# Optimization experiments

Measured on AMD Instinct MI355X. Metric: run time of the kernel, lower is better.

Reference implementation:

```python
import jax, jax.numpy as jnp
import numpy as np
import math

LN_EPS = 1e-5

def layer_norm(x, g, b):
    mu = jnp.mean(x, axis=-1, keepdims=True)
    var = jnp.mean(jnp.square(x - mu), axis=-1, keepdims=True)
    return (x - mu) * jax.lax.rsqrt(var + LN_EPS) * g + b

def positional_encoding(seq_len, d_model):
    pos = jnp.arange(seq_len, dtype=jnp.float32)[:, None]
    div = jnp.exp(jnp.arange(0, d_model, 2, dtype=jnp.float32) * (-math.log(10000.0) / d_model))
    ang = pos * div  # [S, D/2]
    # interleave: even indices sin, odd indices cos
    return jnp.stack([jnp.sin(ang), jnp.cos(ang)], axis=-1).reshape(seq_len, d_model)

def setup_inputs() -> dict:
    key = jax.random.key(0)
    V, D, H, L, F, B, S = 32000, 768, 12, 6, 3072, 4, 1024
    ks = jax.random.split(key, 12)
    s = 0.02
    inp = {
        'tokens': jax.random.randint(ks[0], (B, S), 0, V),
        'emb': jax.random.normal(ks[1], (V, D), jnp.float32) * s,
        'Wq': jax.random.normal(ks[2], (L, D, D), jnp.float32) * s,
        'bq': jnp.zeros((L, D), jnp.float32),
        'Wk': jax.random.normal(ks[3], (L, D, D), jnp.float32) * s,
        'bk': jnp.zeros((L, D), jnp.float32),
        'Wv': jax.random.normal(ks[4], (L, D, D), jnp.float32) * s,
        'bv': jnp.zeros((L, D), jnp.float32),
        'Wo': jax.random.normal(ks[5], (L, D, D), jnp.float32) * s,
        'bo': jnp.zeros((L, D), jnp.float32),
        'W1': jax.random.normal(ks[6], (L, D, F), jnp.float32) * s,
        'b1': jnp.zeros((L, F), jnp.float32),
        'W2': jax.random.normal(ks[7], (L, F, D), jnp.float32) * s,
        'b2': jnp.zeros((L, D), jnp.float32),
        'ln1_g': jnp.ones((L, D), jnp.float32), 'ln1_b': jnp.zeros((L, D), jnp.float32),
        'ln2_g': jnp.ones((L, D), jnp.float32), 'ln2_b': jnp.zeros((L, D), jnp.float32),
        'lnf_g': jnp.ones((D,), jnp.float32), 'lnf_b': jnp.zeros((D,), jnp.float32),
        'head_W': jax.random.normal(ks[8], (V, D), jnp.float32) * s,
    }
    return inp

def gpt_forward(tokens, emb, Wq, bq, Wk, bk, Wv, bv, Wo, bo, W1, b1, W2, b2,
                ln1_g, ln1_b, ln2_g, ln2_b, lnf_g, lnf_b, head_W):
    B, S = tokens.shape
    D = emb.shape[1]
    H = 12
    dk = D // H
    scale = 1.0 / math.sqrt(dk)
    causal = jnp.tril(jnp.ones((S, S), dtype=bool))  # [S,S]

    x = emb[tokens] + positional_encoding(S, D)  # [B,S,D]

    def block(x, p):
        wq, bq_, wk, bk_, wv, bv_, wo, bo_, w1, b1_, w2, b2_, g1, be1, g2, be2 = p
        h = layer_norm(x, g1, be1)
        q = (h @ wq + bq_).reshape(B, S, H, dk)
        k = (h @ wk + bk_).reshape(B, S, H, dk)
        v = (h @ wv + bv_).reshape(B, S, H, dk)
        scores = jnp.einsum('bqhd,bkhd->bhqk', q, k) * scale
        scores = jnp.where(causal, scores, -jnp.inf)
        attn = jax.nn.softmax(scores, axis=-1)
        o = jnp.einsum('bhqk,bkhd->bqhd', attn, v).reshape(B, S, D)
        x = x + o @ wo + bo_
        h2 = layer_norm(x, g2, be2)
        ff = jax.nn.gelu(h2 @ w1 + b1_, approximate=False) @ w2 + b2_
        x = x + ff
        return x, None

    layer_params = (Wq, bq, Wk, bk, Wv, bv, Wo, bo, W1, b1, W2, b2,
                    ln1_g, ln1_b, ln2_g, ln2_b)
    x, _ = jax.lax.scan(block, x, layer_params)
    x = layer_norm(x, lnf_g, lnf_b)
    logits = jnp.einsum('bsd,vd->bsv', x, head_W)  # head bias=False
    return logits

def reference(tokens, emb, Wq, bq, Wk, bk, Wv, bv, Wo, bo, W1, b1, W2, b2,
              ln1_g, ln1_b, ln2_g, ln2_b, lnf_g, lnf_b, head_W):
    return gpt_forward(tokens, emb, Wq, bq, Wk, bk, Wv, bv, Wo, bo, W1, b1, W2, b2,
                       ln1_g, ln1_b, ln2_g, ln2_b, lnf_g, lnf_b, head_W)
```

## Files before the change

kernel.cpp:

```cpp
#include <hip/hip_runtime.h>
#include <hip/hip_bf16.h>
#include <math.h>

#define BB 4
#define SS 1024
#define DD 768
#define HH 12
#define LL 6
#define FF 3072
#define VV 32000
#define DK 64
#define MM (BB * SS)

typedef __attribute__((ext_vector_type(8))) short s8v;
typedef __attribute__((ext_vector_type(4))) float f4v;

__device__ inline unsigned short f2bf_bits(float f) {
    unsigned u = __builtin_bit_cast(unsigned, f);
    unsigned r = (u + 0x7fffu + ((u >> 16) & 1u)) >> 16;
    return (unsigned short)r;
}

__device__ inline void gl_lds16(const void* g, void* l) {
    __builtin_amdgcn_global_load_lds((const __attribute__((address_space(1))) void*)g,
                                     (__attribute__((address_space(3))) void*)l, 16, 0, 0);
}

__global__ void embed_kernel(const int* __restrict__ tokens,
                             const float* __restrict__ emb,
                             float* __restrict__ x) {
    const int row = blockIdx.x;
    const int s = row % SS;
    const int tok = tokens[row];
    const float* er = emb + (size_t)tok * DD;
    float* xr = x + (size_t)row * DD;
    const float neg_ln_base = -logf(10000.0f) / (float)DD;
    for (int d = threadIdx.x; d < DD; d += blockDim.x) {
        int i2 = d & ~1;
        float div = expf((float)i2 * neg_ln_base);
        float ang = (float)s * div;
        float pe = (d & 1) ? cosf(ang) : sinf(ang);
        xr[d] = er[d] + pe;
    }
}

template <int OUTBF>
__global__ __launch_bounds__(256) void ln_kernel(const float* __restrict__ x,
                                                 const float* __restrict__ g,
                                                 const float* __restrict__ b,
                                                 void* __restrict__ outp) {
    const int row = blockIdx.x;
    const float* xr = x + (size_t)row * DD;
    float s = 0.f, s2 = 0.f;
    for (int d = threadIdx.x; d < DD; d += blockDim.x) {
        float v = xr[d];
        s += v; s2 += v * v;
    }
    __shared__ float rs[4], rs2[4];
    for (int off = 32; off; off >>= 1) {
        s  += __shfl_down(s, off);
        s2 += __shfl_down(s2, off);
    }
    const int wid = threadIdx.x >> 6;
    if ((threadIdx.x & 63) == 0) { rs[wid] = s; rs2[wid] = s2; }
    __syncthreads();
    s  = rs[0] + rs[1] + rs[2] + rs[3];
    s2 = rs2[0] + rs2[1] + rs2[2] + rs2[3];
    const float mu = s / (float)DD;
    const float var = s2 / (float)DD - mu * mu;
    const float r = rsqrtf(var + 1e-5f);
    for (int d = threadIdx.x; d < DD; d += blockDim.x) {
        float v = (xr[d] - mu) * r * g[d] + b[d];
        if (OUTBF) ((unsigned short*)outp)[(size_t)row * DD + d] = f2bf_bits(v);
        else       ((float*)outp)[(size_t)row * DD + d] = v;
    }
}

__global__ __launch_bounds__(256) void prep_kernel(const float* __restrict__ Wq,
                                                   const float* __restrict__ Wk,
                                                   const float* __restrict__ Wv,
                                                   const float* __restrict__ Wo,
                                                   const float* __restrict__ W1,
                                                   const float* __restrict__ W2,
                                                   unsigned short* __restrict__ wqkvT,
                                                   unsigned short* __restrict__ woT,
                                                   unsigned short* __restrict__ w1T,
                                                   unsigned short* __restrict__ w2T) {
    const size_t DxD = (size_t)DD * DD, DxF = (size_t)DD * FF;
    const int lid = blockIdx.x / 1728;
    const int id  = blockIdx.x % 1728;
    const float* src; unsigned short* dst; int R, C, t;
    if (id < 432)       { int seg = id / 144; t = id % 144;
                          src = (seg == 0 ? Wq : seg == 1 ? Wk : Wv) + lid * DxD;
                          dst = wqkvT + lid * 3 * DxD + (size_t)seg * DxD; R = DD; C = DD; }
    else if (id < 576)  { t = id - 432; src = Wo + lid * DxD; dst = woT + lid * DxD; R = DD; C = DD; }
    else if (id < 1152) { t = id - 576;  src = W1 + lid * DxF; dst = w1T + lid * DxF; R = DD; C = FF; }
    else                { t = id - 1152; src = W2 + lid * DxF; dst = w2T + lid * DxF; R = FF; C = DD; }
    const int tilesC = C / 64;
    const int r0 = (t / tilesC) * 64, c0 = (t % tilesC) * 64;
    __shared__ float tb[64][65];
    const int lr = threadIdx.x >> 6, lc = threadIdx.x & 63;
    #pragma unroll
    for (int it = 0; it < 16; ++it) {
        int r = it * 4 + lr;
        tb[r][lc] = src[(size_t)(r0 + r) * C + c0 + lc];
    }
    __syncthreads();
    #pragma unroll
    for (int it = 0; it < 16; ++it) {
        int c = it * 4 + lr;
        dst[(size_t)(c0 + c) * R + r0 + lc] = f2bf_bits(tb[lc][c]);
    }
}

__global__ __launch_bounds__(256) void conv_kernel(const float* __restrict__ in,
                                                   unsigned short* __restrict__ out,
                                                   long n4) {
    long i = (long)blockIdx.x * 256 + threadIdx.x;
    if (i < n4) {
        float4 v = ((const float4*)in)[i];
        ushort4 o;
        o.x = f2bf_bits(v.x); o.y = f2bf_bits(v.y);
        o.z = f2bf_bits(v.z); o.w = f2bf_bits(v.w);
        ((ushort4*)out)[i] = o;
    }
}

template <int BM, int BN, int WGM, int WGN, int ACT, int RES, int OUTMODE>
__global__ __launch_bounds__(256) void gemm_mfma(const unsigned short* __restrict__ A,
                                                 const unsigned short* __restrict__ Bt,
                                                 const float* __restrict__ bias,
                                                 const float* res,
                                                 void* Cout, int M, int N, int K,
                                                 const float* biasK, const float* biasV,
                                                 unsigned short* kout, unsigned short* vtout) {
    __shared__ unsigned short As[BM * 32];
    __shared__ unsigned short Bs[BN * 32];
    constexpr int MF = (BM / WGM) / 16;
    constexpr int NF = (BN / WGN) / 16;
    const int tid = threadIdx.x;
    const int bm = blockIdx.y * BM, bn = blockIdx.x * BN;
    const int lane = tid & 63;
    const int wave = tid >> 6;
    const int wr = (wave / WGN) * (BM / WGM);
    const int wc = (wave % WGN) * (BN / WGN);

    f4v acc[MF][NF];
    #pragma unroll
    for (int i = 0; i < MF; i++)
        #pragma unroll
        for (int j = 0; j < NF; j++)
            acc[i][j] = (f4v){0.f, 0.f, 0.f, 0.f};

    const int arow = tid >> 2;
    const int acol = (tid & 3) * 8;
    const int fr = lane & 15;
    const int fk = (lane >> 4) * 8;

    for (int k0 = 0; k0 < K; k0 += 32) {
        #pragma unroll
        for (int i = 0; i < BM / 64; i++)
            gl_lds16(A + (size_t)(bm + i * 64 + arow) * K + k0 + acol,
                     (char*)As + i * 4096 + tid * 16);
        #pragma unroll
        for (int i = 0; i < BN / 64; i++)
            gl_lds16(Bt + (size_t)(bn + i * 64 + arow) * K + k0 + acol,
                     (char*)Bs + i * 4096 + tid * 16);
        __syncthreads();
        s8v af[MF], bf[NF];
        #pragma unroll
        for (int i = 0; i < MF; i++)
            af[i] = *(const s8v*)(As + (wr + i * 16 + fr) * 32 + fk);
        #pragma unroll
        for (int j = 0; j < NF; j++)
            bf[j] = *(const s8v*)(Bs + (wc + j * 16 + fr) * 32 + fk);
        #pragma unroll
        for (int i = 0; i < MF; i++)
            #pragma unroll
            for (int j = 0; j < NF; j++)
                acc[i][j] = __builtin_amdgcn_mfma_f32_16x16x32_bf16(af[i], bf[j], acc[i][j], 0, 0, 0);
        __syncthreads();
    }

    const int r0 = bm + wr + (lane >> 4) * 4;
    const int c0 = bn + wc + fr;
    #pragma unroll
    for (int i = 0; i < MF; i++) {
        const int rb = r0 + i * 16;
        #pragma unroll
        for (int j = 0; j < NF; j++) {
            const int c = c0 + j * 16;
            if (OUTMODE == 3) {
                const int seg = (c >= 1536) ? 2 : (c >= 768 ? 1 : 0);
                const int cc = c - seg * 768;
                const float bb = (seg == 0 ? bias[cc] : seg == 1 ? biasK[cc] : biasV[cc]);
                if (seg < 2) {
                    unsigned short* dst = (seg == 0 ? (unsigned short*)Cout : kout);
                    #pragma unroll
                    for (int q = 0; q < 4; q++)
                        dst[(size_t)(rb + q) * DD + cc] = f2bf_bits(acc[i][j][q] + bb);
                } else {
                    const int b_ = rb / SS, s_ = rb % SS;
                    const int h_ = cc >> 6, dd = cc & 63;
                    ushort4 pk;
                    pk.x = f2bf_bits(acc[i][j][0] + bb);
                    pk.y = f2bf_bits(acc[i][j][1] + bb);
                    pk.z = f2bf_bits(acc[i][j][2] + bb);
                    pk.w = f2bf_bits(acc[i][j][3] + bb);
                    *(ushort4*)(vtout + ((size_t)(b_ * HH + h_) * DK + dd) * SS + s_) = pk;
                }
            } else {
                const float bv = bias ? bias[c] : 0.f;
                #pragma unroll
                for (int q = 0; q < 4; q++) {
                    const int r = rb + q;
                    float v = acc[i][j][q] + bv;
                    if (ACT) v = 0.5f * v * (1.0f + erff(v * 0.70710678118654752f));
                    if (RES) v += res[(size_t)r * N + c];
                    if (OUTMODE == 1) ((unsigned short*)Cout)[(size_t)r * N + c] = f2bf_bits(v);
                    else              ((float*)Cout)[(size_t)r * N + c] = v;
                }
            }
        }
    }
}

__global__ __launch_bounds__(512) void gemm_head(const unsigned short* __restrict__ A,
                                                 const unsigned short* __restrict__ Bt,
                                                 float* __restrict__ C,
                                                 int M, int N, int K) {
    __shared__ unsigned short As[256 * 32];
    __shared__ unsigned short Bs[128 * 32];
    const int tid = threadIdx.x;

    const int f = blockIdx.y * gridDim.x + blockIdx.x;
    const int v = (f & 7) * 500 + (f >> 3);
    int bx, by;
    if (v < 3840) {
        const int bnd = v >> 8;
        const int r = v & 255;
        by = r >> 4;
        bx = bnd * 16 + (r & 15);
    } else {
        const int r = v - 3840;
        by = r / 10;
        bx = 240 + r % 10;
    }
    const int bm = by * 256, bn = bx * 128;

    const int lane = tid & 63;
    const int wave = tid >> 6;
    const int wm = (wave >> 1) * 64;
    const int wn = (wave & 1) * 64;

    f4v acc[4][4];
    #pragma unroll
    for (int i = 0; i < 4; i++)
        #pragma unroll
        for (int j = 0; j < 4; j++)
            acc[i][j] = (f4v){0.f, 0.f, 0.f, 0.f};

    const int arow = tid >> 2;
    const int acol = (tid & 3) * 8;
    const unsigned short* gA0 = A  + (size_t)(bm + arow) * K + acol;
    const unsigned short* gA1 = gA0 + (size_t)128 * K;
    const unsigned short* gB  = Bt + (size_t)(bn + arow) * K + acol;
    char* lA0 = (char*)As + tid * 16;
    char* lA1 = lA0 + 8192;
    char* lB  = (char*)Bs + tid * 16;

    const int fr = lane & 15;
    const int fk = (lane >> 4) * 8;

    for (int k0 = 0; k0 < K; k0 += 32) {
        gl_lds16(gA0 + k0, lA0);
        gl_lds16(gA1 + k0, lA1);
        gl_lds16(gB + k0, lB);
        __syncthreads();
        s8v af[4], bf[4];
        #pragma unroll
        for (int i = 0; i < 4; i++)
            af[i] = *(const s8v*)(As + (wm + i * 16 + fr) * 32 + fk);
        #pragma unroll
        for (int j = 0; j < 4; j++)
            bf[j] = *(const s8v*)(Bs + (wn + j * 16 + fr) * 32 + fk);
        #pragma unroll
        for (int i = 0; i < 4; i++)
            #pragma unroll
            for (int j = 0; j < 4; j++)
                acc[i][j] = __builtin_amdgcn_mfma_f32_16x16x32_bf16(af[i], bf[j], acc[i][j], 0, 0, 0);
        __syncthreads();
    }

    const int r0 = bm + wm + (lane >> 4) * 4;
    const int c0 = bn + wn + fr;
    #pragma unroll
    for (int i = 0; i < 4; i++) {
        #pragma unroll
        for (int j = 0; j < 4; j++) {
            const int c = c0 + j * 16;
            #pragma unroll
            for (int q = 0; q < 4; q++) {
                const int r = r0 + i * 16 + q;
                __builtin_nontemporal_store(acc[i][j][q], &C[(size_t)r * N + c]);
            }
        }
    }
}

__global__ __launch_bounds__(256) void fattn_kernel(const unsigned short* __restrict__ qb,
                                                    const unsigned short* __restrict__ kb,
                                                    const unsigned short* __restrict__ vt,
                                                    unsigned short* __restrict__ o) {
    __shared__ unsigned short Ks[128 * 64];
    __shared__ unsigned short Ps[4][16 * 128];

    const int qt = (int)gridDim.x - 1 - (int)blockIdx.x;
    const int bh = blockIdx.y;
    const int b = bh / HH, h = bh % HH;
    const int tid = threadIdx.x;
    const int lane = tid & 63;
    const int w = tid >> 6;
    const int fr = lane & 15;
    const int g  = lane >> 4;

    const int krow_ = tid >> 3;
    const int kcol = ((tid & 7) ^ (krow_ & 7)) * 8;

    const int q0w = qt * 64 + w * 16;
    s8v qf[2];
    {
        const unsigned short* qrow = qb + (size_t)(b * SS + q0w + fr) * DD + h * DK + g * 8;
        qf[0] = *(const s8v*)(qrow);
        qf[1] = *(const s8v*)(qrow + 32);
    }

    f4v ofr[4];
    #pragma unroll
    for (int dj = 0; dj < 4; dj++) ofr[dj] = (f4v){0.f, 0.f, 0.f, 0.f};
    float mrow[4] = {-1e30f, -1e30f, -1e30f, -1e30f};
    float lrow[4] = {0.f, 0.f, 0.f, 0.f};

    unsigned short* Pw = &Ps[w][0];
    const unsigned short* vbh = vt + (size_t)bh * DK * SS;
    const int ktiles = qt / 2 + 1;

    for (int t = 0; t < ktiles; ++t) {
        const int k0 = t * 128;
        #pragma unroll
        for (int i = 0; i < 4; i++) {
            const int r = i * 32 + krow_;
            gl_lds16(kb + (size_t)(b * SS + k0 + r) * DD + h * DK + kcol,
                     (char*)Ks + i * 4096 + tid * 16);
        }
        __syncthreads();

        const bool diag = (t == ktiles - 1);
        float p[8][4];
        #pragma unroll
        for (int j = 0; j < 8; j++) {
            const char* kbase = (const char*)Ks + (j * 16 + fr) * 128;
            s8v b0 = *(const s8v*)(kbase + ((g * 16)      ^ ((fr & 7) << 4)));
            s8v b1 = *(const s8v*)(kbase + ((64 + g * 16) ^ ((fr & 7) << 4)));
            f4v a = (f4v){0.f, 0.f, 0.f, 0.f};
            a = __builtin_amdgcn_mfma_f32_16x16x32_bf16(qf[0], b0, a, 0, 0, 0);
            a = __builtin_amdgcn_mfma_f32_16x16x32_bf16(qf[1], b1, a, 0, 0, 0);
            #pragma unroll
            for (int pq = 0; pq < 4; pq++) {
                float sv = a[pq] * 0.125f;
                if (diag && (k0 + j * 16 + fr > q0w + g * 4 + pq)) sv = -1e30f;
                p[j][pq] = sv;
            }
        }

        float rmx[4];
        #pragma unroll
        for (int pq = 0; pq < 4; pq++) {
            float v0 = fmaxf(fmaxf(p[0][pq], p[1][pq]), fmaxf(p[2][pq], p[3][pq]));
            float v1 = fmaxf(fmaxf(p[4][pq], p[5][pq]), fmaxf(p[6][pq], p[7][pq]));
            rmx[pq] = fmaxf(v0, v1);
        }
        #pragma unroll
        for (int off = 1; off < 16; off <<= 1)
            #pragma unroll
            for (int pq = 0; pq < 4; pq++)
                rmx[pq] = fmaxf(rmx[pq], __shfl_xor(rmx[pq], off));

        float mnew[4], scf[4], rsum[4];
        #pragma unroll
        for (int pq = 0; pq < 4; pq++) {
            mnew[pq] = fmaxf(mrow[pq], rmx[pq]);
            scf[pq]  = __expf(mrow[pq] - mnew[pq]);
            rsum[pq] = 0.f;
        }
        #pragma unroll
        for (int j = 0; j < 8; j++)
            #pragma unroll
            for (int pq = 0; pq < 4; pq++) {
                float e = __expf(p[j][pq] - mnew[pq]);
                p[j][pq] = e;
                rsum[pq] += e;
            }
        #pragma unroll
        for (int off = 1; off < 16; off <<= 1)
            #pragma unroll
            for (int pq = 0; pq < 4; pq++)
                rsum[pq] += __shfl_xor(rsum[pq], off);
        #pragma unroll
        for (int pq = 0; pq < 4; pq++) {
            lrow[pq] = lrow[pq] * scf[pq] + rsum[pq];
            mrow[pq] = mnew[pq];
        }
        #pragma unroll
        for (int dj = 0; dj < 4; dj++)
            #pragma unroll
            for (int pq = 0; pq < 4; pq++)
                ofr[dj][pq] *= scf[pq];

        #pragma unroll
        for (int j = 0; j < 8; j++)
            #pragma unroll
            for (int pq = 0; pq < 4; pq++) {
                const int r = g * 4 + pq;
                *(unsigned short*)((char*)Pw + r * 256 +
                                   (((j * 16 + fr) * 2) ^ ((r & 7) << 4))) = f2bf_bits(p[j][pq]);
            }

        s8v pa[4];
        #pragma unroll
        for (int ks = 0; ks < 4; ks++)
            pa[ks] = *(const s8v*)((const char*)Pw + fr * 256 +
                                   ((ks * 64 + g * 16) ^ ((fr & 7) << 4)));
        #pragma unroll
        for (int dj = 0; dj < 4; dj++) {
            const unsigned short* vrow = vbh + (size_t)(dj * 16 + fr) * SS + k0;
            #pragma unroll
            for (int ks = 0; ks < 4; ks++) {
                s8v vv = *(const s8v*)(vrow + ks * 32 + g * 8);
                ofr[dj] = __builtin_amdgcn_mfma_f32_16x16x32_bf16(pa[ks], vv, ofr[dj], 0, 0, 0);
            }
        }
        __syncthreads();
    }

    #pragma unroll
    for (int pq = 0; pq < 4; pq++) {
        const float inv = 1.0f / lrow[pq];
        const int row_abs = q0w + g * 4 + pq;
        #pragma unroll
        for (int dj = 0; dj < 4; dj++)
            o[(size_t)(b * SS + row_abs) * DD + h * DK + dj * 16 + fr] =
                f2bf_bits(ofr[dj][pq] * inv);
    }
}

extern "C" void kernel_launch(void* const* d_in, const int* in_sizes, int n_in,
                              void* d_out, int out_size, void* d_ws, size_t ws_size,
                              hipStream_t stream) {
    const int*   tokens = (const int*)d_in[0];
    const float* emb    = (const float*)d_in[1];
    const float* Wq     = (const float*)d_in[2];
    const float* bq     = (const float*)d_in[3];
    const float* Wk     = (const float*)d_in[4];
    const float* bk     = (const float*)d_in[5];
    const float* Wv     = (const float*)d_in[6];
    const float* bv     = (const float*)d_in[7];
    const float* Wo     = (const float*)d_in[8];
    const float* bo     = (const float*)d_in[9];
    const float* W1     = (const float*)d_in[10];
    const float* b1     = (const float*)d_in[11];
    const float* W2     = (const float*)d_in[12];
    const float* b2     = (const float*)d_in[13];
    const float* ln1_g  = (const float*)d_in[14];
    const float* ln1_b  = (const float*)d_in[15];
    const float* ln2_g  = (const float*)d_in[16];
    const float* ln2_b  = (const float*)d_in[17];
    const float* lnf_g  = (const float*)d_in[18];
    const float* lnf_b  = (const float*)d_in[19];
    const float* headW  = (const float*)d_in[20];
    float* out = (float*)d_out;
    (void)in_sizes; (void)n_in; (void)out_size; (void)ws_size;

    const size_t MD  = (size_t)MM * DD;
    const size_t MF_ = (size_t)MM * FF;
    const size_t DxD = (size_t)DD * DD;
    const size_t DxF = (size_t)DD * FF;
    const size_t HWs = (size_t)VV * DD;

    char* p = (char*)d_ws;
    float*          x     = (float*)p;          p += MD * 4;
    unsigned short* qb    = (unsigned short*)p; p += MD * 2;
    unsigned short* kbuf  = (unsigned short*)p; p += MD * 2;
    unsigned short* vtb   = (unsigned short*)p; p += MD * 2;
    unsigned short* ao    = (unsigned short*)p; p += MD * 2;
    unsigned short* h     = (unsigned short*)p; p += MD * 2;
    unsigned short* mid   = (unsigned short*)p; p += MF_ * 2;
    unsigned short* wqkvT = (unsigned short*)p; p += 6 * 3 * DxD * 2;
    unsigned short* woT   = (unsigned short*)p; p += 6 * DxD * 2;
    unsigned short* w1T   = (unsigned short*)p; p += 6 * DxF * 2;
    unsigned short* w2T   = (unsigned short*)p; p += 6 * DxF * 2;
    unsigned short* hw    = (unsigned short*)p; p += HWs * 2;

    embed_kernel<<<MM, 256, 0, stream>>>(tokens, emb, x);
    conv_kernel<<<(int)((HWs / 4 + 255) / 256), 256, 0, stream>>>(headW, hw, (long)(HWs / 4));
    prep_kernel<<<6 * 1728, 256, 0, stream>>>(Wq, Wk, Wv, Wo, W1, W2, wqkvT, woT, w1T, w2T);

    const dim3 gQKV(2304 / 128, MM / 128);
    const dim3 gDn(DD / 128, MM / 64);
    const dim3 gF(FF / 128, MM / 128);
    const dim3 gHead(VV / 128, MM / 256);
    const dim3 gA(SS / 64, BB * HH);

    for (int l = 0; l < LL; l++) {
        ln_kernel<1><<<MM, 256, 0, stream>>>(x, ln1_g + l * DD, ln1_b + l * DD, h);
        gemm_mfma<128, 128, 2, 2, 0, 0, 3><<<gQKV, 256, 0, stream>>>(
            h, wqkvT + (size_t)l * 3 * DxD, bq + l * DD, nullptr, qb, MM, 2304, DD,
            bk + l * DD, bv + l * DD, kbuf, vtb);
        fattn_kernel<<<gA, 256, 0, stream>>>(qb, kbuf, vtb, ao);
        gemm_mfma<64, 128, 1, 4, 0, 1, 0><<<gDn, 256, 0, stream>>>(
            ao, woT + (size_t)l * DxD, bo + l * DD, x, x, MM, DD, DD,
            nullptr, nullptr, nullptr, nullptr);
        ln_kernel<1><<<MM, 256, 0, stream>>>(x, ln2_g + l * DD, ln2_b + l * DD, h);
        gemm_mfma<128, 128, 2, 2, 1, 0, 1><<<gF, 256, 0, stream>>>(
            h, w1T + (size_t)l * DxF, b1 + l * FF, nullptr, mid, MM, FF, DD,
            nullptr, nullptr, nullptr, nullptr);
        gemm_mfma<64, 128, 1, 4, 0, 1, 0><<<gDn, 256, 0, stream>>>(
            mid, w2T + (size_t)l * DxF, b2 + l * DD, x, x, MM, DD, FF,
            nullptr, nullptr, nullptr, nullptr);
    }

    ln_kernel<1><<<MM, 256, 0, stream>>>(x, lnf_g, lnf_b, h);
    gemm_head<<<gHead, 512, 0, stream>>>(h, hw, out, MM, VV, DD);
}
```

Before: 1.837 ms.

## Deepen GEMM K-step to 64 with XOR-swizzled LDS, warp-per-row layernorm, attention setprio

The generic and head GEMMs now stage 64-wide K slices per iteration into XOR-swizzled LDS rows. This halves the number of barrier pairs per K loop and aims to avoid LDS bank conflicts on the fragment reads, at the cost of doubling shared memory per block. LayerNorm is reworked so each wavefront handles one row with float4 loads kept in registers and a shuffle-only reduction, with four rows per block and no LDS or barrier. The attention MFMA sections are wrapped in s_setprio to raise wave priority during matrix work.

```diff
diff --git a/kernel.cpp b/kernel.cpp
--- a/kernel.cpp
+++ b/kernel.cpp
@@ -49,30 +49,45 @@
                                                  const float* __restrict__ g,
                                                  const float* __restrict__ b,
                                                  void* __restrict__ outp) {
-    const int row = blockIdx.x;
+    const int row = blockIdx.x * 4 + (threadIdx.x >> 6);
+    const int lane = threadIdx.x & 63;
     const float* xr = x + (size_t)row * DD;
+
+    float4 v[3];
     float s = 0.f, s2 = 0.f;
-    for (int d = threadIdx.x; d < DD; d += blockDim.x) {
-        float v = xr[d];
-        s += v; s2 += v * v;
-    }
-    __shared__ float rs[4], rs2[4];
+    #pragma unroll
+    for (int j = 0; j < 3; j++) {
+        v[j] = *(const float4*)(xr + j * 256 + lane * 4);
+        s  += v[j].x + v[j].y + v[j].z + v[j].w;
+        s2 += v[j].x * v[j].x + v[j].y * v[j].y + v[j].z * v[j].z + v[j].w * v[j].w;
+    }
+    #pragma unroll
     for (int off = 32; off; off >>= 1) {
-        s  += __shfl_down(s, off);
-        s2 += __shfl_down(s2, off);
-    }
-    const int wid = threadIdx.x >> 6;
-    if ((threadIdx.x & 63) == 0) { rs[wid] = s; rs2[wid] = s2; }
-    __syncthreads();
-    s  = rs[0] + rs[1] + rs[2] + rs[3];
-    s2 = rs2[0] + rs2[1] + rs2[2] + rs2[3];
+        s  += __shfl_xor(s, off);
+        s2 += __shfl_xor(s2, off);
+    }
     const float mu = s / (float)DD;
     const float var = s2 / (float)DD - mu * mu;
     const float r = rsqrtf(var + 1e-5f);
-    for (int d = threadIdx.x; d < DD; d += blockDim.x) {
-        float v = (xr[d] - mu) * r * g[d] + b[d];
-        if (OUTBF) ((unsigned short*)outp)[(size_t)row * DD + d] = f2bf_bits(v);
-        else       ((float*)outp)[(size_t)row * DD + d] = v;
+
+    #pragma unroll
+    for (int j = 0; j < 3; j++) {
+        const int c = j * 256 + lane * 4;
+        const float4 gv = *(const float4*)(g + c);
+        const float4 bv = *(const float4*)(b + c);
+        float o0 = (v[j].x - mu) * r * gv.x + bv.x;
+        float o1 = (v[j].y - mu) * r * gv.y + bv.y;
+        float o2 = (v[j].z - mu) * r * gv.z + bv.z;
+        float o3 = (v[j].w - mu) * r * gv.w + bv.w;
+        if (OUTBF) {
+            ushort4 o;
+            o.x = f2bf_bits(o0); o.y = f2bf_bits(o1);
+            o.z = f2bf_bits(o2); o.w = f2bf_bits(o3);
+            *(ushort4*)((unsigned short*)outp + (size_t)row * DD + c) = o;
+        } else {
+            float4 o = {o0, o1, o2, o3};
+            *(float4*)((float*)outp + (size_t)row * DD + c) = o;
+        }
     }
 }
 
@@ -134,8 +149,8 @@
                                                  void* Cout, int M, int N, int K,
                                                  const float* biasK, const float* biasV,
                                                  unsigned short* kout, unsigned short* vtout) {
-    __shared__ unsigned short As[BM * 32];
-    __shared__ unsigned short Bs[BN * 32];
+    __shared__ unsigned short As[BM * 64];
+    __shared__ unsigned short Bs[BN * 64];
     constexpr int MF = (BM / WGM) / 16;
     constexpr int NF = (BN / WGN) / 16;
     const int tid = threadIdx.x;
@@ -152,33 +167,47 @@
         for (int j = 0; j < NF; j++)
             acc[i][j] = (f4v){0.f, 0.f, 0.f, 0.f};
 
-    const int arow = tid >> 2;
-    const int acol = (tid & 3) * 8;
+    const int srow = tid >> 3;
+    const int sch  = tid & 7;
+    const int scol = (sch ^ (srow & 7)) * 8;
     const int fr = lane & 15;
-    const int fk = (lane >> 4) * 8;
-
-    for (int k0 = 0; k0 < K; k0 += 32) {
-        #pragma unroll
-        for (int i = 0; i < BM / 64; i++)
-            gl_lds16(A + (size_t)(bm + i * 64 + arow) * K + k0 + acol,
-                     (char*)As + i * 4096 + tid * 16);
-        #pragma unroll
-        for (int i = 0; i < BN / 64; i++)
-            gl_lds16(Bt + (size_t)(bn + i * 64 + arow) * K + k0 + acol,
-                     (char*)Bs + i * 4096 + tid * 16);
+    const int g  = lane >> 4;
+
+    for (int k0 = 0; k0 < K; k0 += 64) {
+        #pragma unroll
+        for (int p = 0; p < BM / 32; p++)
+            gl_lds16(A + (size_t)(bm + p * 32 + srow) * K + k0 + scol,
+                     (char*)As + (p * 32 + srow) * 128 + sch * 16);
+        #pragma unroll
+        for (int p = 0; p < BN / 32; p++)
+            gl_lds16(Bt + (size_t)(bn + p * 32 + srow) * K + k0 + scol,
+                     (char*)Bs + (p * 32 + srow) * 128 + sch * 16);
         __syncthreads();
-        s8v af[MF], bf[NF];
-        #pragma unroll
-        for (int i = 0; i < MF; i++)
-            af[i] = *(const s8v*)(As + (wr + i * 16 + fr) * 32 + fk);
-        #pragma unroll
-        for (int j = 0; j < NF; j++)
-            bf[j] = *(const s8v*)(Bs + (wc + j * 16 + fr) * 32 + fk);
-        #pragma unroll
-        for (int i = 0; i < MF; i++)
+
+        s8v bf[NF][2];
+        #pragma unroll
+        for (int j = 0; j < NF; j++) {
+            const int row = wc + j * 16 + fr;
+            #pragma unroll
+            for (int ks = 0; ks < 2; ks++)
+                bf[j][ks] = *(const s8v*)((const char*)Bs + row * 128 +
+                                          ((ks * 64 + g * 16) ^ ((row & 7) << 4)));
+        }
+        #pragma unroll
+        for (int i = 0; i < MF; i++) {
+            const int row = wr + i * 16 + fr;
+            s8v af[2];
+            #pragma unroll
+            for (int ks = 0; ks < 2; ks++)
+                af[ks] = *(const s8v*)((const char*)As + row * 128 +
+                                       ((ks * 64 + g * 16) ^ ((row & 7) << 4)));
             #pragma unroll
             for (int j = 0; j < NF; j++)
-                acc[i][j] = __builtin_amdgcn_mfma_f32_16x16x32_bf16(af[i], bf[j], acc[i][j], 0, 0, 0);
+                #pragma unroll
+                for (int ks = 0; ks < 2; ks++)
+                    acc[i][j] = __builtin_amdgcn_mfma_f32_16x16x32_bf16(af[ks], bf[j][ks],
+                                                                        acc[i][j], 0, 0, 0);
+        }
         __syncthreads();
     }
 
@@ -229,29 +258,24 @@
                                                  const unsigned short* __restrict__ Bt,
                                                  float* __restrict__ C,
                                                  int M, int N, int K) {
-    __shared__ unsigned short As[256 * 32];
-    __shared__ unsigned short Bs[128 * 32];
+    __shared__ unsigned short As[256 * 64];
+    __shared__ unsigned short Bs[128 * 64];
     const int tid = threadIdx.x;
 
     const int f = blockIdx.y * gridDim.x + blockIdx.x;
     const int v = (f & 7) * 500 + (f >> 3);
     int bx, by;
-    if (v < 3840) {
-        const int bnd = v >> 8;
-        const int r = v & 255;
-        by = r >> 4;
-        bx = bnd * 16 + (r & 15);
-    } else {
-        const int r = v - 3840;
-        by = r / 10;
-        bx = 240 + r % 10;
-    }
+    if (v < 3840) { const int bnd = v >> 8; const int r = v & 255;
+                    by = r >> 4; bx = bnd * 16 + (r & 15); }
+    else          { const int r = v - 3840; by = r / 10; bx = 240 + r % 10; }
     const int bm = by * 256, bn = bx * 128;
 
     const int lane = tid & 63;
     const int wave = tid >> 6;
     const int wm = (wave >> 1) * 64;
     const int wn = (wave & 1) * 64;
+    const int fr = lane & 15;
+    const int g  = lane >> 4;
 
     f4v acc[4][4];
     #pragma unroll
@@ -260,39 +284,49 @@
         for (int j = 0; j < 4; j++)
             acc[i][j] = (f4v){0.f, 0.f, 0.f, 0.f};
 
-    const int arow = tid >> 2;
-    const int acol = (tid & 3) * 8;
-    const unsigned short* gA0 = A  + (size_t)(bm + arow) * K + acol;
-    const unsigned short* gA1 = gA0 + (size_t)128 * K;
-    const unsigned short* gB  = Bt + (size_t)(bn + arow) * K + acol;
-    char* lA0 = (char*)As + tid * 16;
-    char* lA1 = lA0 + 8192;
-    char* lB  = (char*)Bs + tid * 16;
-
-    const int fr = lane & 15;
-    const int fk = (lane >> 4) * 8;
-
-    for (int k0 = 0; k0 < K; k0 += 32) {
-        gl_lds16(gA0 + k0, lA0);
-        gl_lds16(gA1 + k0, lA1);
-        gl_lds16(gB + k0, lB);
+    const int srow = tid >> 3;
+    const int sch  = tid & 7;
+    const int scol = (sch ^ (srow & 7)) * 8;
+
+    for (int k0 = 0; k0 < K; k0 += 64) {
+        #pragma unroll
+        for (int p = 0; p < 4; p++)
+            gl_lds16(A + (size_t)(bm + p * 64 + srow) * K + k0 + scol,
+                     (char*)As + (p * 64 + srow) * 128 + sch * 16);
+        #pragma unroll
+        for (int p = 0; p < 2; p++)
+            gl_lds16(Bt + (size_t)(bn + p * 64 + srow) * K + k0 + scol,
+                     (char*)Bs + (p * 64 + srow) * 128 + sch * 16);
         __syncthreads();
-        s8v af[4], bf[4];
-        #pragma unroll
-        for (int i = 0; i < 4; i++)
-            af[i] = *(const s8v*)(As + (wm + i * 16 + fr) * 32 + fk);
-        #pragma unroll
-        for (int j = 0; j < 4; j++)
-            bf[j] = *(const s8v*)(Bs + (wn + j * 16 + fr) * 32 + fk);
-        #pragma unroll
-        for (int i = 0; i < 4; i++)
+
+        s8v bf[4][2];
+        #pragma unroll
+        for (int j = 0; j < 4; j++) {
+            const int row = wn + j * 16 + fr;
+            #pragma unroll
+            for (int ks = 0; ks < 2; ks++)
+                bf[j][ks] = *(const s8v*)((const char*)Bs + row * 128 +
+                                          ((ks * 64 + g * 16) ^ ((row & 7) << 4)));
+        }
+        #pragma unroll
+        for (int i = 0; i < 4; i++) {
+            const int row = wm + i * 16 + fr;
+            s8v af[2];
+            #pragma unroll
+            for (int ks = 0; ks < 2; ks++)
+                af[ks] = *(const s8v*)((const char*)As + row * 128 +
+                                       ((ks * 64 + g * 16) ^ ((row & 7) << 4)));
             #pragma unroll
             for (int j = 0; j < 4; j++)
-                acc[i][j] = __builtin_amdgcn_mfma_f32_16x16x32_bf16(af[i], bf[j], acc[i][j], 0, 0, 0);
+                #pragma unroll
+                for (int ks = 0; ks < 2; ks++)
+                    acc[i][j] = __builtin_amdgcn_mfma_f32_16x16x32_bf16(af[ks], bf[j][ks],
+                                                                        acc[i][j], 0, 0, 0);
+        }
         __syncthreads();
     }
 
-    const int r0 = bm + wm + (lane >> 4) * 4;
+    const int r0 = bm + wm + g * 4;
     const int c0 = bn + wn + fr;
     #pragma unroll
     for (int i = 0; i < 4; i++) {
@@ -357,6 +391,7 @@
 
         const bool diag = (t == ktiles - 1);
         float p[8][4];
+        __builtin_amdgcn_s_setprio(1);
         #pragma unroll
         for (int j = 0; j < 8; j++) {
             const char* kbase = (const char*)Ks + (j * 16 + fr) * 128;
@@ -372,6 +407,7 @@
                 p[j][pq] = sv;
             }
         }
+        __builtin_amdgcn_s_setprio(0);
 
         float rmx[4];
         #pragma unroll
@@ -431,6 +467,7 @@
         for (int ks = 0; ks < 4; ks++)
             pa[ks] = *(const s8v*)((const char*)Pw + fr * 256 +
                                    ((ks * 64 + g * 16) ^ ((fr & 7) << 4)));
+        __builtin_amdgcn_s_setprio(1);
         #pragma unroll
         for (int dj = 0; dj < 4; dj++) {
             const unsigned short* vrow = vbh + (size_t)(dj * 16 + fr) * SS + k0;
@@ -440,6 +477,7 @@
                 ofr[dj] = __builtin_amdgcn_mfma_f32_16x16x32_bf16(pa[ks], vv, ofr[dj], 0, 0, 0);
             }
         }
+        __builtin_amdgcn_s_setprio(0);
         __syncthreads();
     }
 
@@ -510,9 +548,10 @@
     const dim3 gF(FF / 128, MM / 128);
     const dim3 gHead(VV / 128, MM / 256);
     const dim3 gA(SS / 64, BB * HH);
+    const int  gLN = MM / 4;
 
     for (int l = 0; l < LL; l++) {
-        ln_kernel<1><<<MM, 256, 0, stream>>>(x, ln1_g + l * DD, ln1_b + l * DD, h);
+        ln_kernel<1><<<gLN, 256, 0, stream>>>(x, ln1_g + l * DD, ln1_b + l * DD, h);
         gemm_mfma<128, 128, 2, 2, 0, 0, 3><<<gQKV, 256, 0, stream>>>(
             h, wqkvT + (size_t)l * 3 * DxD, bq + l * DD, nullptr, qb, MM, 2304, DD,
             bk + l * DD, bv + l * DD, kbuf, vtb);
@@ -520,7 +559,7 @@
         gemm_mfma<64, 128, 1, 4, 0, 1, 0><<<gDn, 256, 0, stream>>>(
             ao, woT + (size_t)l * DxD, bo + l * DD, x, x, MM, DD, DD,
             nullptr, nullptr, nullptr, nullptr);
-        ln_kernel<1><<<MM, 256, 0, stream>>>(x, ln2_g + l * DD, ln2_b + l * DD, h);
+        ln_kernel<1><<<gLN, 256, 0, stream>>>(x, ln2_g + l * DD, ln2_b + l * DD, h);
         gemm_mfma<128, 128, 2, 2, 1, 0, 1><<<gF, 256, 0, stream>>>(
             h, w1T + (size_t)l * DxF, b1 + l * FF, nullptr, mid, MM, FF, DD,
             nullptr, nullptr, nullptr, nullptr);
@@ -529,6 +568,6 @@
             nullptr, nullptr, nullptr, nullptr);
     }
 
-    ln_kernel<1><<<MM, 256, 0, stream>>>(x, lnf_g, lnf_b, h);
+    ln_kernel<1><<<gLN, 256, 0, stream>>>(x, lnf_g, lnf_b, h);
     gemm_head<<<gHead, 512, 0, stream>>>(h, hw, out, MM, VV, DD);
 }
```

Result: slower. 1.993 ms (+8.5%).
